# Performance work log

Measured on AMD Instinct MI355X. Metric: run time of the kernel, lower is better.

The kernel has to match this reference:

```python
import jax, jax.numpy as jnp
import numpy as np

HEADS = 16
DIM_HEAD = 64
DIM = 1024
INNER = HEADS * DIM_HEAD  # 1024


def setup_inputs() -> dict:
    key = jax.random.key(0)
    ks = jax.random.split(key, 8)
    B, N, M = 4, 2048, 2048
    x = jax.random.normal(ks[0], (B, N, DIM), dtype=jnp.float32)
    context = jax.random.normal(ks[1], (B, M, DIM), dtype=jnp.float32)
    x_mask = (jax.random.uniform(ks[2], (B, N)) > 0.1).astype(jnp.float32)
    context_mask = (jax.random.uniform(ks[3], (B, M)) > 0.1).astype(jnp.float32)
    s = 0.02
    Wq = jax.random.normal(ks[4], (DIM, INNER), dtype=jnp.float32) * s
    Wkv = jax.random.normal(ks[5], (DIM, 2 * INNER), dtype=jnp.float32) * s
    Wo = jax.random.normal(ks[6], (INNER, DIM), dtype=jnp.float32) * s
    bo = jnp.zeros((DIM,), dtype=jnp.float32)
    return {"x": x, "context": context, "x_mask": x_mask,
            "context_mask": context_mask, "Wq": Wq, "Wkv": Wkv, "Wo": Wo, "bo": bo}


def _split_heads(t):
    b, n, _ = t.shape
    return t.reshape(b, n, HEADS, DIM_HEAD).transpose(0, 2, 1, 3)  # b h n d


def reference(x, context, x_mask, context_mask, Wq, Wkv, Wo, bo):
    scale = DIM_HEAD ** -0.5
    q = _split_heads(x @ Wq)                       # b h n d
    kv = context @ Wkv
    k = _split_heads(kv[..., :INNER])              # b h m d
    v = _split_heads(kv[..., INNER:])              # b h m d
    dots = jnp.einsum('bhnd,bhmd->bhnm', q, k) * scale
    # attn_bias = 1 - x_mask ⊗ context_mask; masked where isclose(attn_bias, 1)
    prod = x_mask[:, None, :, None] * context_mask[:, None, None, :]  # b 1 n m
    masked = jnp.isclose(1.0 - prod, 1.0)          # b 1 n m, broadcast over heads
    dots = jnp.where(masked, -jnp.inf, dots)       # b h n m
    # rows with no valid key: zero the whole row before softmax
    valid = jnp.any(~masked, axis=-1, keepdims=True)  # b 1 n 1
    dots = jnp.where(valid, dots, 0.0)
    attn = jax.nn.softmax(dots, axis=-1)
    attn = jnp.where(valid, attn, 0.0)
    out = jnp.einsum('bhnm,bhmd->bhnd', attn, v)
    b, h, n, d = out.shape
    out = out.transpose(0, 2, 1, 3).reshape(b, n, h * d)
    return out @ Wo + bo
```

## Files before the change

### kernel.cpp

```cpp
#include <hip/hip_runtime.h>

#define DEVI __device__ __forceinline__

typedef __attribute__((ext_vector_type(4))) float f32x4;
typedef __attribute__((ext_vector_type(8))) _Float16 f16x8;
typedef __attribute__((ext_vector_type(2))) _Float16 f16x2;
typedef __attribute__((ext_vector_type(4))) unsigned u32x4;

#if __has_builtin(__builtin_amdgcn_exp2f)
#define EXP2F __builtin_amdgcn_exp2f
#else
#define EXP2F exp2f
#endif

DEVI ushort f2h(float f) {
  _Float16 h = (_Float16)f;
  return __builtin_bit_cast(ushort, h);
}

DEVI unsigned pkrtz(float a, float b) {
  return __builtin_bit_cast(unsigned, __builtin_amdgcn_cvt_pkrtz(a, b));
}

DEVI float dot2acc(unsigned pk, float acc) {
#if __has_builtin(__builtin_amdgcn_fdot2)
  f16x2 one2 = {(_Float16)1.0f, (_Float16)1.0f};
  return __builtin_amdgcn_fdot2(__builtin_bit_cast(f16x2, pk), one2, acc, false);
#else
  f16x2 v = __builtin_bit_cast(f16x2, pk);
  return acc + (float)v[0] + (float)v[1];
#endif
}

DEVI void gload_lds16(const void* g, void* l) {
  typedef const unsigned int GlobU __attribute__((address_space(1)));
  typedef unsigned int LdsU __attribute__((address_space(3)));
  __builtin_amdgcn_global_load_lds((GlobU*)g, (LdsU*)l, 16, 0, 0);
}

__global__ __launch_bounds__(256) void cast_f16_kernel(
    const float4* __restrict__ x, const float4* __restrict__ ctx,
    ushort4* __restrict__ xo, ushort4* __restrict__ co) {
  int i = blockIdx.x * 256 + threadIdx.x;
  const float4* src;
  ushort4* dst;
  int j;
  if (i < 2097152) { src = x; dst = xo; j = i; }
  else             { src = ctx; dst = co; j = i - 2097152; }
  float4 v = src[j];
  ushort4 o;
  o.x = f2h(v.x); o.y = f2h(v.y); o.z = f2h(v.z); o.w = f2h(v.w);
  dst[j] = o;
}

__global__ __launch_bounds__(256) void transpose_cast_kernel(
    const float* __restrict__ Wq, const float* __restrict__ Wkv,
    const float* __restrict__ Wo, ushort* __restrict__ WqT,
    ushort* __restrict__ WkvT, ushort* __restrict__ WoT) {
  __shared__ ushort tile[64][65];
  int bx = blockIdx.x;
  const float* in; ushort* out; int C, cb;
  if (bx < 16)      { in = Wq;  out = WqT;  C = 1024; cb = bx * 64; }
  else if (bx < 48) { in = Wkv; out = WkvT; C = 2048; cb = (bx - 16) * 64; }
  else              { in = Wo;  out = WoT;  C = 1024; cb = (bx - 48) * 64; }
  const int R = 1024;
  int rb = blockIdx.y * 64;
  int t = threadIdx.x;
  int c4 = (t & 15) * 4, r0 = t >> 4;
#pragma unroll
  for (int i = 0; i < 4; i++) {
    int r = r0 + i * 16;
    float4 v = *(const float4*)(in + (size_t)(rb + r) * C + cb + c4);
    tile[r][c4 + 0] = f2h(v.x);
    tile[r][c4 + 1] = f2h(v.y);
    tile[r][c4 + 2] = f2h(v.z);
    tile[r][c4 + 3] = f2h(v.w);
  }
  __syncthreads();
#pragma unroll
  for (int i = 0; i < 4; i++) {
    int rr = r0 + i * 16;
    ushort4 o;
    o.x = tile[c4 + 0][rr]; o.y = tile[c4 + 1][rr];
    o.z = tile[c4 + 2][rr]; o.w = tile[c4 + 3][rr];
    *(ushort4*)(out + (size_t)(cb + rr) * R + rb + c4) = o;
  }
}

DEVI void gemm_stage(const ushort* __restrict__ A, const ushort* __restrict__ Bt,
                     int K, int rowbase, int colbase, int tid, int wave,
                     ushort* AsC, ushort* BsC, int kk) {
#pragma unroll
  for (int i = 0; i < 2; i++) {
    int f = i * 256 + tid;
    int r = f >> 2;
    int c = (f & 3) ^ (r & 3);
    gload_lds16(A + (size_t)(rowbase + r) * K + (kk + c * 8),
                (char*)AsC + (size_t)(i * 256 + wave * 64) * 16);
    gload_lds16(Bt + (size_t)(colbase + r) * K + (kk + c * 8),
                (char*)BsC + (size_t)(i * 256 + wave * 64) * 16);
  }
}

DEVI void gemm_core(const ushort* __restrict__ A, const ushort* __restrict__ Bt,
                    const int K, int rowbase, int colbase, int tid,
                    ushort* As, ushort* Bs, f32x4 acc[4][4]) {
  const int lane = tid & 63, wave = tid >> 6;
  const int quad = lane >> 4, ln = lane & 15;
  const int wrow = (wave >> 1) * 64, wcol = (wave & 1) * 64;

  gemm_stage(A, Bt, K, rowbase, colbase, tid, wave, As, Bs, 0);
  gemm_stage(A, Bt, K, rowbase, colbase, tid, wave, As + 4096, Bs + 4096, 32);

  for (int k0 = 0; k0 < K; k0 += 32) {
    const int cur = (k0 >> 5) & 1;
    ushort* AsC = As + cur * 4096;
    ushort* BsC = Bs + cur * 4096;

    if (k0 + 32 < K) asm volatile("s_waitcnt vmcnt(4)" ::: "memory");
    else             asm volatile("s_waitcnt vmcnt(0)" ::: "memory");
    asm volatile("s_barrier" ::: "memory");

    f16x8 a[4], b[4];
#pragma unroll
    for (int mt = 0; mt < 4; mt++) {
      int r = wrow + mt * 16 + ln;
      a[mt] = *(const f16x8*)(AsC + ((size_t)r * 4 + (quad ^ (r & 3))) * 8);
    }
#pragma unroll
    for (int nt = 0; nt < 4; nt++) {
      int r = wcol + nt * 16 + ln;
      b[nt] = *(const f16x8*)(BsC + ((size_t)r * 4 + (quad ^ (r & 3))) * 8);
    }
#pragma unroll
    for (int mt = 0; mt < 4; mt++)
#pragma unroll
      for (int nt = 0; nt < 4; nt++)
        acc[mt][nt] = __builtin_amdgcn_mfma_f32_16x16x32_f16(a[mt], b[nt], acc[mt][nt], 0, 0, 0);

    asm volatile("s_barrier" ::: "memory");
    if (k0 + 64 < K)
      gemm_stage(A, Bt, K, rowbase, colbase, tid, wave, AsC, BsC, k0 + 64);
  }
}

__global__ __launch_bounds__(256, 3) void qkv_gemm(
    const ushort* __restrict__ xb, const ushort* __restrict__ cb,
    const ushort* __restrict__ WqT, const ushort* __restrict__ WkvT,
    ushort* __restrict__ Qo, ushort* __restrict__ Ko, ushort* __restrict__ Vo) {
  __shared__ ushort As[2 * 128 * 32];
  __shared__ ushort Bs[2 * 128 * 32];
  const int tid = threadIdx.x;
  const int lane = tid & 63, wave = tid >> 6;
  const int quad = lane >> 4, ln = lane & 15;
  const int cy = blockIdx.y;
  const bool isQ = cy < 8;
  const int colbase = (isQ ? cy : cy - 8) * 128;
  const int rowbase = blockIdx.x * 128;
  const int wrow = (wave >> 1) * 64, wcol = (wave & 1) * 64;
  f32x4 acc[4][4] = {};
  gemm_core(isQ ? xb : cb, isQ ? WqT : WkvT, 1024, rowbase, colbase, tid, As, Bs, acc);

  if (isQ) {
    const float qs = 0.18033688011112042f;
#pragma unroll
    for (int nt = 0; nt < 4; nt++) {
      int col = colbase + wcol + nt * 16 + ln;
      int h = col >> 6, d = col & 63;
#pragma unroll
      for (int mt = 0; mt < 4; mt++) {
        int row = rowbase + wrow + mt * 16 + quad * 4;
        int bb = row >> 11, n = row & 2047;
        uint2 pv;
        pv.x = pkrtz(acc[mt][nt][0] * qs, acc[mt][nt][1] * qs);
        pv.y = pkrtz(acc[mt][nt][2] * qs, acc[mt][nt][3] * qs);
        *(uint2*)(Qo + (((size_t)bb * 16 + h) * 64 + d) * 2048 + n) = pv;
      }
    }
  } else {
    bool isK = (colbase < 1024);
#pragma unroll
    for (int nt = 0; nt < 4; nt++) {
      int col = colbase + wcol + nt * 16 + ln;
#pragma unroll
      for (int mt = 0; mt < 4; mt++) {
        int row = rowbase + wrow + mt * 16 + quad * 4;
        int bb = row >> 11, m = row & 2047;
        if (isK) {
          int h = col >> 6, d = col & 63;
#pragma unroll
          for (int r = 0; r < 4; r++)
            Ko[(((size_t)bb * 16 + h) * 2048 + (m + r)) * 64 + d] = f2h(acc[mt][nt][r]);
        } else {
          int c2 = col - 1024;
          int h = c2 >> 6, d = c2 & 63;
          uint2 pv;
          pv.x = pkrtz(acc[mt][nt][0], acc[mt][nt][1]);
          pv.y = pkrtz(acc[mt][nt][2], acc[mt][nt][3]);
          *(uint2*)(Vo + (((size_t)bb * 16 + h) * 64 + d) * 2048 + m) = pv;
        }
      }
    }
  }
}

__global__ __launch_bounds__(256, 3) void out_gemm(
    const ushort* __restrict__ A, const ushort* __restrict__ Bt,
    float* __restrict__ C, const float* __restrict__ bias) {
  __shared__ ushort As[2 * 128 * 32];
  __shared__ ushort Bs[2 * 128 * 32];
  const int tid = threadIdx.x;
  const int lane = tid & 63, wave = tid >> 6;
  const int quad = lane >> 4, ln = lane & 15;
  const int colbase = blockIdx.y * 128, rowbase = blockIdx.x * 128;
  const int wrow = (wave >> 1) * 64, wcol = (wave & 1) * 64;
  f32x4 acc[4][4] = {};
  gemm_core(A, Bt, 1024, rowbase, colbase, tid, As, Bs, acc);
#pragma unroll
  for (int nt = 0; nt < 4; nt++) {
    int col = colbase + wcol + nt * 16 + ln;
    float bv = bias[col];
#pragma unroll
    for (int mt = 0; mt < 4; mt++) {
      int row = rowbase + wrow + mt * 16 + quad * 4;
#pragma unroll
      for (int r = 0; r < 4; r++)
        C[(size_t)(row + r) * 1024 + col] = acc[mt][nt][r] + bv;
    }
  }
}

__global__ __launch_bounds__(512, 4) void attn_kernel(
    const ushort* __restrict__ QT, const ushort* __restrict__ K,
    const ushort* __restrict__ VT, const float* __restrict__ xmask,
    const float* __restrict__ cmask, ushort* __restrict__ O) {
  __shared__ ushort Ks[2][64 * 64];
  __shared__ ushort Vs[2][64 * 64];
  __shared__ float CMB[2048];
  const int tid = threadIdx.x, lane = tid & 63, wave = tid >> 6;
  const int quad = lane >> 4, ln = lane & 15;
  const int bid = blockIdx.x;
  const int qb = bid >> 6, bh6 = bid & 63, h = bh6 & 15, b = bh6 >> 4;
  const size_t bh = (size_t)b * 16 + h;
  const ushort* QTbh = QT + bh * (64 * 2048);
  const ushort* Kbh = K + bh * (2048 * 64);
  const ushort* Vbh = VT + bh * (64 * 2048);
  const int q0 = qb * 256 + wave * 32;

  {
    float4 c0 = *(const float4*)(cmask + b * 2048 + tid * 4);
    float4 b0;
    b0.x = fmaf(c0.x, 3.0e4f, -3.0e4f); b0.y = fmaf(c0.y, 3.0e4f, -3.0e4f);
    b0.z = fmaf(c0.z, 3.0e4f, -3.0e4f); b0.w = fmaf(c0.w, 3.0e4f, -3.0e4f);
    *(float4*)(CMB + tid * 4) = b0;
  }

  f16x8 qf[2][2];
#pragma unroll
  for (int qt = 0; qt < 2; qt++)
#pragma unroll
    for (int kc = 0; kc < 2; kc++) {
      int q = q0 + qt * 16 + ln;
#pragma unroll
      for (int j = 0; j < 8; j++)
        qf[qt][kc][j] = __builtin_bit_cast(_Float16,
            (unsigned short)QTbh[(size_t)(kc * 32 + quad * 8 + j) * 2048 + q]);
    }

  float xm[2];
#pragma unroll
  for (int qt = 0; qt < 2; qt++) xm[qt] = xmask[b * 2048 + q0 + qt * 16 + ln];

  __syncthreads();

  const int sr = tid >> 3;
  const int sc = (tid & 7) ^ (sr & 7);
  const int srp = (sr & 32) | ((sr & 12) << 1) | ((sr & 16) >> 2) | (sr & 3);

#pragma unroll
  for (int t = 0; t < 2; t++) {
    gload_lds16(Kbh + (size_t)(t * 64 + srp) * 64 + sc * 8, (char*)Ks[t] + (size_t)tid * 16);
    gload_lds16(Vbh + (size_t)sr * 2048 + (t * 64 + sc * 8), (char*)Vs[t] + (size_t)tid * 16);
  }

  f32x4 o[4][2] = {};
  float lpart[2] = {0.f, 0.f};

  for (int kb = 0; kb < 32; kb++) {
    const int cur = kb & 1;
    const int m0 = kb * 64;
    const ushort* KsC = Ks[cur];
    const ushort* VsC = Vs[cur];

    if (kb < 31) asm volatile("s_waitcnt vmcnt(2)" ::: "memory");
    else         asm volatile("s_waitcnt vmcnt(0)" ::: "memory");
    asm volatile("s_barrier" ::: "memory");

    f32x4 bias4[4];
#pragma unroll
    for (int kt = 0; kt < 4; kt++)
      bias4[kt] = *(const f32x4*)(CMB + m0 + (kt >> 1) * 32 + quad * 8 + (kt & 1) * 4);

    f32x4 s[4][2];
#pragma unroll
    for (int kt = 0; kt < 4; kt++)
#pragma unroll
      for (int qt = 0; qt < 2; qt++) s[kt][qt] = bias4[kt];
#pragma unroll
    for (int kc = 0; kc < 2; kc++) {
#pragma unroll
      for (int kt = 0; kt < 4; kt++) {
        int r = kt * 16 + ln;
        f16x8 ka = *(const f16x8*)(KsC + ((size_t)r * 8 + ((kc * 4 + quad) ^ (r & 7))) * 8);
#pragma unroll
        for (int qt = 0; qt < 2; qt++)
          s[kt][qt] = __builtin_amdgcn_mfma_f32_16x16x32_f16(ka, qf[qt][kc], s[kt][qt], 0, 0, 0);
      }
    }

#pragma unroll
    for (int kc = 0; kc < 2; kc++) {
      f16x8 pf[2];
#pragma unroll
      for (int qt = 0; qt < 2; qt++) {
        f32x4 sA = s[kc * 2 + 0][qt];
        f32x4 sB = s[kc * 2 + 1][qt];
        u32x4 u;
        u[0] = pkrtz(EXP2F(sA[0]), EXP2F(sA[1]));
        u[1] = pkrtz(EXP2F(sA[2]), EXP2F(sA[3]));
        u[2] = pkrtz(EXP2F(sB[0]), EXP2F(sB[1]));
        u[3] = pkrtz(EXP2F(sB[2]), EXP2F(sB[3]));
        lpart[qt] = dot2acc(u[0], lpart[qt]);
        lpart[qt] = dot2acc(u[1], lpart[qt]);
        lpart[qt] = dot2acc(u[2], lpart[qt]);
        lpart[qt] = dot2acc(u[3], lpart[qt]);
        pf[qt] = __builtin_bit_cast(f16x8, u);
      }
#pragma unroll
      for (int dt = 0; dt < 4; dt++) {
        int r = dt * 16 + ln;
        f16x8 va = *(const f16x8*)(VsC + ((size_t)r * 8 + ((kc * 4 + quad) ^ (r & 7))) * 8);
#pragma unroll
        for (int qt = 0; qt < 2; qt++)
          o[dt][qt] = __builtin_amdgcn_mfma_f32_16x16x32_f16(va, pf[qt], o[dt][qt], 0, 0, 0);
      }
    }

    asm volatile("s_barrier" ::: "memory");
    if (kb < 30) {
      const int m2 = m0 + 128;
      gload_lds16(Kbh + (size_t)(m2 + srp) * 64 + sc * 8, (char*)Ks[cur] + (size_t)tid * 16);
      gload_lds16(Vbh + (size_t)sr * 2048 + (m2 + sc * 8), (char*)Vs[cur] + (size_t)tid * 16);
    }
  }

#pragma unroll
  for (int qt = 0; qt < 2; qt++) {
    float l = lpart[qt];
    l += __shfl_xor(l, 16, 64);
    l += __shfl_xor(l, 32, 64);
    float inv = (xm[qt] != 0.f && l > 0.f) ? (1.f / l) : 0.f;
    int n = q0 + qt * 16 + ln;
    ushort* ob = O + ((size_t)(b * 2048 + n) * 16 + h) * 64;
#pragma unroll
    for (int dt = 0; dt < 4; dt++) {
      uint2 pv;
      pv.x = pkrtz(o[dt][qt][0] * inv, o[dt][qt][1] * inv);
      pv.y = pkrtz(o[dt][qt][2] * inv, o[dt][qt][3] * inv);
      *(uint2*)(ob + dt * 16 + quad * 4) = pv;
    }
  }
}

extern "C" void kernel_launch(void* const* d_in, const int* in_sizes, int n_in,
                              void* d_out, int out_size, void* d_ws, size_t ws_size,
                              hipStream_t stream) {
  const float* x   = (const float*)d_in[0];
  const float* ctx = (const float*)d_in[1];
  const float* xm  = (const float*)d_in[2];
  const float* cm  = (const float*)d_in[3];
  const float* Wq  = (const float*)d_in[4];
  const float* Wkv = (const float*)d_in[5];
  const float* Wo  = (const float*)d_in[6];
  const float* bo  = (const float*)d_in[7];

  char* ws = (char*)d_ws;
  const size_t MB = 1024 * 1024;
  ushort* xb   = (ushort*)(ws + 0);
  ushort* cb   = (ushort*)(ws + 16 * MB);
  ushort* WqT  = (ushort*)(ws + 32 * MB);
  ushort* WkvT = (ushort*)(ws + 34 * MB);
  ushort* WoT  = (ushort*)(ws + 38 * MB);
  ushort* QTb  = (ushort*)(ws + 40 * MB);
  ushort* Kb   = (ushort*)(ws + 56 * MB);
  ushort* VTb  = (ushort*)(ws + 72 * MB);
  ushort* Ob   = xb;

  cast_f16_kernel<<<16384, 256, 0, stream>>>((const float4*)x, (const float4*)ctx,
                                             (ushort4*)xb, (ushort4*)cb);
  transpose_cast_kernel<<<dim3(64, 16), 256, 0, stream>>>(Wq, Wkv, Wo, WqT, WkvT, WoT);
  qkv_gemm<<<dim3(64, 24), 256, 0, stream>>>(xb, cb, WqT, WkvT, QTb, Kb, VTb);
  attn_kernel<<<512, 512, 0, stream>>>(QTb, Kb, VTb, xm, cm, Ob);
  out_gemm<<<dim3(64, 8), 256, 0, stream>>>(Ob, WoT, (float*)d_out, bo);
}
```

Before: 306.6 us.

## Halve attention block waves and give each wave 64 query rows

The attention kernel now runs 4 waves per block instead of 8, with each wave handling 64 queries instead of 32. Each K/V fragment read from LDS is therefore reused across four query tiles, which lowers LDS traffic per MFMA. The smaller thread count means each thread issues twice as many global-to-LDS loads, so the wait count is raised to match. The costs are more accumulator registers per thread and fewer waves sharing the same staged tile, which may reduce occupancy and latency hiding.

```diff
diff --git a/kernel.cpp b/kernel.cpp
--- a/kernel.cpp
+++ b/kernel.cpp
@@ -230,7 +230,7 @@
   }
 }
 
-__global__ __launch_bounds__(512, 4) void attn_kernel(
+__global__ __launch_bounds__(256, 2) void attn_kernel(
     const ushort* __restrict__ QT, const ushort* __restrict__ K,
     const ushort* __restrict__ VT, const float* __restrict__ xmask,
     const float* __restrict__ cmask, ushort* __restrict__ O) {
@@ -245,19 +245,22 @@
   const ushort* QTbh = QT + bh * (64 * 2048);
   const ushort* Kbh = K + bh * (2048 * 64);
   const ushort* Vbh = VT + bh * (64 * 2048);
-  const int q0 = qb * 256 + wave * 32;
+  const int q0 = qb * 256 + wave * 64;
 
   {
-    float4 c0 = *(const float4*)(cmask + b * 2048 + tid * 4);
-    float4 b0;
-    b0.x = fmaf(c0.x, 3.0e4f, -3.0e4f); b0.y = fmaf(c0.y, 3.0e4f, -3.0e4f);
-    b0.z = fmaf(c0.z, 3.0e4f, -3.0e4f); b0.w = fmaf(c0.w, 3.0e4f, -3.0e4f);
-    *(float4*)(CMB + tid * 4) = b0;
-  }
-
-  f16x8 qf[2][2];
-#pragma unroll
-  for (int qt = 0; qt < 2; qt++)
+#pragma unroll
+    for (int i = 0; i < 2; i++) {
+      float4 c0 = *(const float4*)(cmask + b * 2048 + tid * 8 + i * 4);
+      float4 b0;
+      b0.x = fmaf(c0.x, 3.0e4f, -3.0e4f); b0.y = fmaf(c0.y, 3.0e4f, -3.0e4f);
+      b0.z = fmaf(c0.z, 3.0e4f, -3.0e4f); b0.w = fmaf(c0.w, 3.0e4f, -3.0e4f);
+      *(float4*)(CMB + tid * 8 + i * 4) = b0;
+    }
+  }
+
+  f16x8 qf[4][2];
+#pragma unroll
+  for (int qt = 0; qt < 4; qt++)
 #pragma unroll
     for (int kc = 0; kc < 2; kc++) {
       int q = q0 + qt * 16 + ln;
@@ -267,24 +270,27 @@
             (unsigned short)QTbh[(size_t)(kc * 32 + quad * 8 + j) * 2048 + q]);
     }
 
-  float xm[2];
-#pragma unroll
-  for (int qt = 0; qt < 2; qt++) xm[qt] = xmask[b * 2048 + q0 + qt * 16 + ln];
+  float xm[4];
+#pragma unroll
+  for (int qt = 0; qt < 4; qt++) xm[qt] = xmask[b * 2048 + q0 + qt * 16 + ln];
 
   __syncthreads();
 
-  const int sr = tid >> 3;
-  const int sc = (tid & 7) ^ (sr & 7);
-  const int srp = (sr & 32) | ((sr & 12) << 1) | ((sr & 16) >> 2) | (sr & 3);
-
 #pragma unroll
   for (int t = 0; t < 2; t++) {
-    gload_lds16(Kbh + (size_t)(t * 64 + srp) * 64 + sc * 8, (char*)Ks[t] + (size_t)tid * 16);
-    gload_lds16(Vbh + (size_t)sr * 2048 + (t * 64 + sc * 8), (char*)Vs[t] + (size_t)tid * 16);
-  }
-
-  f32x4 o[4][2] = {};
-  float lpart[2] = {0.f, 0.f};
+#pragma unroll
+    for (int i = 0; i < 2; i++) {
+      int f = i * 256 + tid;
+      int r = f >> 3;
+      int c = (f & 7) ^ (r & 7);
+      int rp = (r & 32) | ((r & 12) << 1) | ((r & 16) >> 2) | (r & 3);
+      gload_lds16(Kbh + (size_t)(t * 64 + rp) * 64 + c * 8, (char*)Ks[t] + (size_t)f * 16);
+      gload_lds16(Vbh + (size_t)r * 2048 + (t * 64 + c * 8), (char*)Vs[t] + (size_t)f * 16);
+    }
+  }
+
+  f32x4 o[4][4] = {};
+  float lpart[4] = {0.f, 0.f, 0.f, 0.f};
 
   for (int kb = 0; kb < 32; kb++) {
     const int cur = kb & 1;
@@ -292,7 +298,7 @@
     const ushort* KsC = Ks[cur];
     const ushort* VsC = Vs[cur];
 
-    if (kb < 31) asm volatile("s_waitcnt vmcnt(2)" ::: "memory");
+    if (kb < 31) asm volatile("s_waitcnt vmcnt(4)" ::: "memory");
     else         asm volatile("s_waitcnt vmcnt(0)" ::: "memory");
     asm volatile("s_barrier" ::: "memory");
 
@@ -301,11 +307,11 @@
     for (int kt = 0; kt < 4; kt++)
       bias4[kt] = *(const f32x4*)(CMB + m0 + (kt >> 1) * 32 + quad * 8 + (kt & 1) * 4);
 
-    f32x4 s[4][2];
+    f32x4 s[4][4];
 #pragma unroll
     for (int kt = 0; kt < 4; kt++)
 #pragma unroll
-      for (int qt = 0; qt < 2; qt++) s[kt][qt] = bias4[kt];
+      for (int qt = 0; qt < 4; qt++) s[kt][qt] = bias4[kt];
 #pragma unroll
     for (int kc = 0; kc < 2; kc++) {
 #pragma unroll
@@ -313,16 +319,16 @@
         int r = kt * 16 + ln;
         f16x8 ka = *(const f16x8*)(KsC + ((size_t)r * 8 + ((kc * 4 + quad) ^ (r & 7))) * 8);
 #pragma unroll
-        for (int qt = 0; qt < 2; qt++)
+        for (int qt = 0; qt < 4; qt++)
           s[kt][qt] = __builtin_amdgcn_mfma_f32_16x16x32_f16(ka, qf[qt][kc], s[kt][qt], 0, 0, 0);
       }
     }
 
 #pragma unroll
     for (int kc = 0; kc < 2; kc++) {
-      f16x8 pf[2];
-#pragma unroll
-      for (int qt = 0; qt < 2; qt++) {
+      f16x8 pf[4];
+#pragma unroll
+      for (int qt = 0; qt < 4; qt++) {
         f32x4 sA = s[kc * 2 + 0][qt];
         f32x4 sB = s[kc * 2 + 1][qt];
         u32x4 u;
@@ -341,7 +347,7 @@
         int r = dt * 16 + ln;
         f16x8 va = *(const f16x8*)(VsC + ((size_t)r * 8 + ((kc * 4 + quad) ^ (r & 7))) * 8);
 #pragma unroll
-        for (int qt = 0; qt < 2; qt++)
+        for (int qt = 0; qt < 4; qt++)
           o[dt][qt] = __builtin_amdgcn_mfma_f32_16x16x32_f16(va, pf[qt], o[dt][qt], 0, 0, 0);
       }
     }
@@ -349,13 +355,20 @@
     asm volatile("s_barrier" ::: "memory");
     if (kb < 30) {
       const int m2 = m0 + 128;
-      gload_lds16(Kbh + (size_t)(m2 + srp) * 64 + sc * 8, (char*)Ks[cur] + (size_t)tid * 16);
-      gload_lds16(Vbh + (size_t)sr * 2048 + (m2 + sc * 8), (char*)Vs[cur] + (size_t)tid * 16);
-    }
-  }
-
-#pragma unroll
-  for (int qt = 0; qt < 2; qt++) {
+#pragma unroll
+      for (int i = 0; i < 2; i++) {
+        int f = i * 256 + tid;
+        int r = f >> 3;
+        int c = (f & 7) ^ (r & 7);
+        int rp = (r & 32) | ((r & 12) << 1) | ((r & 16) >> 2) | (r & 3);
+        gload_lds16(Kbh + (size_t)(m2 + rp) * 64 + c * 8, (char*)Ks[cur] + (size_t)f * 16);
+        gload_lds16(Vbh + (size_t)r * 2048 + (m2 + c * 8), (char*)Vs[cur] + (size_t)f * 16);
+      }
+    }
+  }
+
+#pragma unroll
+  for (int qt = 0; qt < 4; qt++) {
     float l = lpart[qt];
     l += __shfl_xor(l, 16, 64);
     l += __shfl_xor(l, 32, 64);
@@ -400,6 +413,6 @@
                                              (ushort4*)xb, (ushort4*)cb);
   transpose_cast_kernel<<<dim3(64, 16), 256, 0, stream>>>(Wq, Wkv, Wo, WqT, WkvT, WoT);
   qkv_gemm<<<dim3(64, 24), 256, 0, stream>>>(xb, cb, WqT, WkvT, QTb, Kb, VTb);
-  attn_kernel<<<512, 512, 0, stream>>>(QTb, Kb, VTb, xm, cm, Ob);
+  attn_kernel<<<512, 256, 0, stream>>>(QTb, Kb, VTb, xm, cm, Ob);
   out_gemm<<<dim3(64, 8), 256, 0, stream>>>(Ob, WoT, (float*)d_out, bo);
 }
```

New measurement: 297.2 us. 3.0% less time.
